# Kernel optimization log

Hardware: AMD Instinct MI355X
Metric: run time of the kernel (lower is better)

The kernel has to match this reference:

```python
import jax, jax.numpy as jnp
import numpy as np

N_NODES = 100000
N_EDGES = 1600000
IN_F = 128
OUT_F = 64
BN_EPS = 1e-5


def setup_inputs() -> dict:
    key = jax.random.key(0)
    ks = jax.random.split(key, 6)
    feature = jax.random.normal(ks[0], (N_NODES, IN_F), dtype=jnp.float32)
    src = jax.random.randint(ks[1], (N_EDGES,), 0, N_NODES, dtype=jnp.int32)
    dst = jax.random.randint(ks[2], (N_EDGES,), 0, N_NODES, dtype=jnp.int32)
    W = jax.random.normal(ks[3], (IN_F, OUT_F), dtype=jnp.float32) * 0.05
    b = jnp.zeros((OUT_F,), dtype=jnp.float32)
    res_W = jax.random.normal(ks[4], (IN_F, OUT_F), dtype=jnp.float32) * 0.05
    res_b = jnp.zeros((OUT_F,), dtype=jnp.float32)
    gamma = jnp.ones((OUT_F,), dtype=jnp.float32)
    beta = jnp.zeros((OUT_F,), dtype=jnp.float32)
    return {"feature": feature, "src": src, "dst": dst, "W": W, "b": b,
            "res_W": res_W, "res_b": res_b, "gamma": gamma, "beta": beta,
            "idx": 0}


def _gcn_layer(feature, src, dst, W, b, res_W, res_b, gamma, beta):
    n = feature.shape[0]
    ones = jnp.ones_like(src, dtype=feature.dtype)
    # DGL norm='both': src-side uses out-degree, dst-side uses in-degree,
    # degrees clamped to min 1 (allow_zero_in_degree=True).
    out_deg = jax.ops.segment_sum(ones, src, num_segments=n)
    in_deg = jax.ops.segment_sum(ones, dst, num_segments=n)
    norm_src = jax.lax.rsqrt(jnp.maximum(out_deg, 1.0))  # [N]
    norm_dst = jax.lax.rsqrt(jnp.maximum(in_deg, 1.0))   # [N]

    # in_feats (128) > out_feats (64): DGL multiplies by W before aggregation.
    h = (feature * norm_src[:, None]) @ W                 # [N, OUT_F]
    agg = jax.ops.segment_sum(h[src], dst, num_segments=n)  # [N, OUT_F]
    conv = jax.nn.relu(agg * norm_dst[:, None] + b)

    # residual connection: activation(Linear(feature))
    res = jax.nn.relu(feature @ res_W + res_b)
    y = conv + res

    # BatchNorm1d (training mode, biased variance)
    mean = jnp.mean(y, axis=0)
    var = jnp.mean(jnp.square(y - mean), axis=0)
    y = (y - mean) * jax.lax.rsqrt(var + BN_EPS) * gamma + beta
    return y


def reference(feature, src, dst, W, b, res_W, res_b, gamma, beta, idx):
    # idx == 0 -> dropout branch is skipped (eval-deterministic reference)
    return _gcn_layer(feature, src, dst, W, b, res_W, res_b, gamma, beta)
```

## Files before the change

### kernel.cpp

```cpp
#include <hip/hip_runtime.h>
#include <hip/hip_fp16.h>

#define NCOL 64
#define KDIM 128
#define NB 512
#define CH 2048

typedef short bf16x8 __attribute__((ext_vector_type(8)));
typedef float f32x4 __attribute__((ext_vector_type(4)));
typedef float f32x2 __attribute__((ext_vector_type(2)));

__device__ __forceinline__ unsigned short f2bf(float f) {
    unsigned int u = __float_as_uint(f);
    return (unsigned short)((u + 0x7fffu + ((u >> 16) & 1u)) >> 16);
}

__global__ __launch_bounds__(256) void coarse_hist(const int* __restrict__ dst,
                                                   int* __restrict__ bcnt, int E) {
    __shared__ int lh[NB];
    int tid = threadIdx.x;
    for (int i = tid; i < NB; i += 256) lh[i] = 0;
    __syncthreads();
    int i = blockIdx.x * blockDim.x + tid;
    int stride = gridDim.x * blockDim.x;
    for (int e = i; e < E; e += stride)
        atomicAdd(&lh[dst[e] >> 8], 1);
    __syncthreads();
    for (int k = tid; k < NB; k += 256) {
        int c = lh[k];
        if (c) atomicAdd(&bcnt[k], c);
    }
}

__global__ __launch_bounds__(256) void bucket_scan(const int* __restrict__ bcnt,
                                                   int* __restrict__ bbase, int* __restrict__ bcur,
                                                   int* __restrict__ row_start, int N, int E) {
    __shared__ int wsum[8];
    int tid = threadIdx.x, lane = tid & 63, wv = tid >> 6;
    int a = bcnt[tid], b = bcnt[tid + 256];
    int ia = a, ib = b;
#pragma unroll
    for (int off = 1; off < 64; off <<= 1) {
        int t = __shfl_up(ia, off); if (lane >= off) ia += t;
        int u = __shfl_up(ib, off); if (lane >= off) ib += u;
    }
    if (lane == 63) { wsum[wv] = ia; wsum[4 + wv] = ib; }
    __syncthreads();
    if (tid == 0) { int run = 0; for (int i = 0; i < 8; ++i) { int t = wsum[i]; wsum[i] = run; run += t; } }
    __syncthreads();
    int ea = wsum[wv] + ia - a;
    int eb = wsum[4 + wv] + ib - b;
    bbase[tid] = ea; bcur[tid] = ea;
    bbase[tid + 256] = eb; bcur[tid + 256] = eb;
    if (tid == 0) row_start[N] = E;
}

__global__ __launch_bounds__(256) void partition_kernel(
    const int* __restrict__ src, const int* __restrict__ dst,
    int* __restrict__ bcur, unsigned int* __restrict__ pk,
    int* __restrict__ outcnt, int E) {
    __shared__ int hist[NB];
    __shared__ int lbase[NB];
    __shared__ int gbase[NB];
    __shared__ int lcur[NB];
    __shared__ uint2 sp[CH];
    __shared__ int wsum[8];

    int tid = threadIdx.x, lane = tid & 63, wv = tid >> 6;
    int c0 = blockIdx.x * CH;
    int cnt = min(CH, E - c0);

    for (int i = tid; i < NB; i += 256) hist[i] = 0;
    __syncthreads();
    for (int i = tid; i < cnt; i += 256)
        atomicAdd(&hist[dst[c0 + i] >> 8], 1);
    __syncthreads();

    {
        int a = hist[tid], b = hist[tid + 256];
        int ia = a, ib = b;
#pragma unroll
        for (int off = 1; off < 64; off <<= 1) {
            int t = __shfl_up(ia, off); if (lane >= off) ia += t;
            int u = __shfl_up(ib, off); if (lane >= off) ib += u;
        }
        if (lane == 63) { wsum[wv] = ia; wsum[4 + wv] = ib; }
        __syncthreads();
        if (tid == 0) { int run = 0; for (int i = 0; i < 8; ++i) { int t = wsum[i]; wsum[i] = run; run += t; } }
        __syncthreads();
        lbase[tid] = wsum[wv] + ia - a;
        lbase[tid + 256] = wsum[4 + wv] + ib - b;
    }
    __syncthreads();

    for (int k = tid; k < NB; k += 256) {
        int c = hist[k];
        gbase[k] = c ? atomicAdd(&bcur[k], c) : 0;
        lcur[k] = lbase[k];
    }
    __syncthreads();

    for (int i = tid; i < cnt; i += 256) {
        int s = src[c0 + i], d = dst[c0 + i];
        atomicAdd(&outcnt[s], 1);
        int p = atomicAdd(&lcur[d >> 8], 1);
        sp[p] = make_uint2((unsigned)s, (unsigned)d);
    }
    __syncthreads();

    for (int i = tid; i < cnt; i += 256) {
        uint2 p = sp[i];
        int k = (int)(p.y >> 8);
        pk[gbase[k] + (i - lbase[k])] = ((p.y & 255u) << 17) | p.x;
    }
}

__global__ __launch_bounds__(256) void fine_kernel(
    const unsigned int* __restrict__ pk, const int* __restrict__ bbase,
    int* __restrict__ row_start, int* __restrict__ ssrc, int E, int nbuck, int N) {
    __shared__ int hist[256];
    __shared__ int cur[256];
    __shared__ int wsum[4];
    int k = blockIdx.x;
    int tid = threadIdx.x, lane = tid & 63, wv = tid >> 6;
    int b0 = bbase[k];
    int b1 = (k + 1 < nbuck) ? bbase[k + 1] : E;

    hist[tid] = 0;
    __syncthreads();
    for (int i = b0 + tid; i < b1; i += 256)
        atomicAdd(&hist[pk[i] >> 17], 1);
    __syncthreads();

    int x = hist[tid], inc = x;
#pragma unroll
    for (int off = 1; off < 64; off <<= 1) {
        int t = __shfl_up(inc, off); if (lane >= off) inc += t;
    }
    if (lane == 63) wsum[wv] = inc;
    __syncthreads();
    if (tid == 0) { int run = 0; for (int i = 0; i < 4; ++i) { int t = wsum[i]; wsum[i] = run; run += t; } }
    __syncthreads();
    int excl = wsum[wv] + inc - x;

    int d = (k << 8) + tid;
    if (d < N) row_start[d] = b0 + excl;
    cur[tid] = b0 + excl;
    __syncthreads();

    for (int i = b0 + tid; i < b1; i += 256) {
        unsigned int p = pk[i];
        int pos = atomicAdd(&cur[p >> 17], 1);
        ssrc[pos] = (int)(p & 0x1FFFFu);
    }
}

__global__ __launch_bounds__(256) void matmul_mfma(
    const float* __restrict__ feat, const float* __restrict__ W,
    const float* __restrict__ RW, const float* __restrict__ res_b,
    const int* __restrict__ outcnt,
    unsigned int* __restrict__ hb8, float* __restrict__ y, int N) {
    __shared__ bf16x8 Bf[2048];
    int tid = threadIdx.x;
    for (int idx = tid; idx < 2048; idx += 256) {
        int mat = idx >> 10;
        int kc = (idx >> 8) & 3;
        int ct = (idx >> 6) & 3;
        int l = idx & 63;
        const float* Wp = mat ? RW : W;
        int kbase = kc * 32 + (l >> 4) * 8;
        int col = ct * 16 + (l & 15);
        bf16x8 t;
#pragma unroll
        for (int j = 0; j < 8; ++j)
            t[j] = (short)f2bf(Wp[(size_t)(kbase + j) * NCOL + col]);
        Bf[idx] = t;
    }
    __syncthreads();

    int lane = tid & 63;
    int wid = tid >> 6;
    int ntiles = (N + 15) >> 4;
    int tile = blockIdx.x * 4 + wid;
    if (tile >= ntiles) return;
    int c16 = lane & 15, kg = lane >> 4;

    float rbv[4];
#pragma unroll
    for (int ct = 0; ct < 4; ++ct) rbv[ct] = res_b[ct * 16 + c16];

    int tb = tile << 4;
    f32x4 acch[4], accr[4];
#pragma unroll
    for (int ct = 0; ct < 4; ++ct) {
        acch[ct] = (f32x4){0.f, 0.f, 0.f, 0.f};
        accr[ct] = (f32x4){0.f, 0.f, 0.f, 0.f};
    }

    int arow = tb + c16; if (arow >= N) arow = N - 1;
    const float* fp = feat + (size_t)arow * KDIM + kg * 8;
#pragma unroll
    for (int kc = 0; kc < 4; ++kc) {
        float4 a0 = *(const float4*)(fp + kc * 32);
        float4 a1 = *(const float4*)(fp + kc * 32 + 4);
        bf16x8 af;
        af[0] = (short)f2bf(a0.x); af[1] = (short)f2bf(a0.y);
        af[2] = (short)f2bf(a0.z); af[3] = (short)f2bf(a0.w);
        af[4] = (short)f2bf(a1.x); af[5] = (short)f2bf(a1.y);
        af[6] = (short)f2bf(a1.z); af[7] = (short)f2bf(a1.w);
#pragma unroll
        for (int ct = 0; ct < 4; ++ct) {
            acch[ct] = __builtin_amdgcn_mfma_f32_16x16x32_bf16(
                af, Bf[(kc * 4 + ct) * 64 + lane], acch[ct], 0, 0, 0);
            accr[ct] = __builtin_amdgcn_mfma_f32_16x16x32_bf16(
                af, Bf[1024 + (kc * 4 + ct) * 64 + lane], accr[ct], 0, 0, 0);
        }
    }

    float nrm[4];
#pragma unroll
    for (int r = 0; r < 4; ++r) {
        int rw = tb + kg * 4 + r; if (rw >= N) rw = N - 1;
        nrm[r] = rsqrtf(fmaxf((float)outcnt[rw], 1.0f));
    }
#pragma unroll
    for (int r = 0; r < 4; ++r) {
        int row = tb + kg * 4 + r;
        if (row < N) {
            unsigned int p = 0;
            p = (unsigned int)__builtin_amdgcn_cvt_pk_fp8_f32(
                    acch[0][r] * nrm[r], acch[1][r] * nrm[r], (int)p, false);
            p = (unsigned int)__builtin_amdgcn_cvt_pk_fp8_f32(
                    acch[2][r] * nrm[r], acch[3][r] * nrm[r], (int)p, true);
#pragma unroll
            for (int ct = 0; ct < 4; ++ct)
                y[(size_t)row * NCOL + ct * 16 + c16] = fmaxf(accr[ct][r] + rbv[ct], 0.0f);
            hb8[(size_t)row * 16 + c16] = p;
        }
    }
}

#define GATHER_ROW_STEP(eBase, eEnd, A0, A1, A2, A3)                                   \
    {                                                                                   \
        int e0 = (eBase) + e4, e1 = e0 + 4, e2 = e0 + 8, e3 = e0 + 12;                  \
        int i0 = (e0 < (eEnd)) ? ssrc[e0] : -1;                                         \
        int i1 = (e1 < (eEnd)) ? ssrc[e1] : -1;                                         \
        int i2 = (e2 < (eEnd)) ? ssrc[e2] : -1;                                         \
        int i3 = (e3 < (eEnd)) ? ssrc[e3] : -1;                                         \
        unsigned int v0 = (i0 >= 0) ? hb8[(size_t)i0 * 16 + dw] : 0u;                   \
        unsigned int v1 = (i1 >= 0) ? hb8[(size_t)i1 * 16 + dw] : 0u;                   \
        unsigned int v2 = (i2 >= 0) ? hb8[(size_t)i2 * 16 + dw] : 0u;                   \
        unsigned int v3 = (i3 >= 0) ? hb8[(size_t)i3 * 16 + dw] : 0u;                   \
        f32x2 l0 = __builtin_amdgcn_cvt_pk_f32_fp8((int)v0, false);                     \
        f32x2 h0 = __builtin_amdgcn_cvt_pk_f32_fp8((int)v0, true);                      \
        f32x2 l1 = __builtin_amdgcn_cvt_pk_f32_fp8((int)v1, false);                     \
        f32x2 h1 = __builtin_amdgcn_cvt_pk_f32_fp8((int)v1, true);                      \
        f32x2 l2 = __builtin_amdgcn_cvt_pk_f32_fp8((int)v2, false);                     \
        f32x2 h2 = __builtin_amdgcn_cvt_pk_f32_fp8((int)v2, true);                      \
        f32x2 l3 = __builtin_amdgcn_cvt_pk_f32_fp8((int)v3, false);                     \
        f32x2 h3 = __builtin_amdgcn_cvt_pk_f32_fp8((int)v3, true);                      \
        A0 += (l0[0] + l1[0]) + (l2[0] + l3[0]);                                        \
        A1 += (l0[1] + l1[1]) + (l2[1] + l3[1]);                                        \
        A2 += (h0[0] + h1[0]) + (h2[0] + h3[0]);                                        \
        A3 += (h0[1] + h1[1]) + (h2[1] + h3[1]);                                        \
    }

__global__ __launch_bounds__(256) void gather_kernel(
    const int* __restrict__ row_start, const int* __restrict__ ssrc,
    const unsigned int* __restrict__ hb8, const float* __restrict__ b,
    float* __restrict__ y, float* __restrict__ stats, int N) {
    int tid = threadIdx.x, lane = tid & 63, wid = tid >> 6;
    int e4 = lane >> 4, dw = lane & 15;
    int rowSel = e4 >> 1;
    int colLo = ((e4 & 1) << 5) + dw;
    int wave = blockIdx.x * 4 + wid;
    int nwaves = gridDim.x * 4;

    float bcLo = b[colLo], bcHi = b[colLo + 16];
    float bnLo = 0.f, bnHi = 0.f, bnsqLo = 0.f, bnsqHi = 0.f;

    for (int d0 = wave * 2; d0 < N; d0 += 2 * nwaves) {
        int d1 = d0 + 1;
        int a0 = row_start[d0], a1 = row_start[d0 + 1];
        int b0e = 0, b1e = 0;
        if (d1 < N) { b0e = a1; b1e = row_start[d1 + 1]; }

        float A0 = 0.f, A1 = 0.f, A2 = 0.f, A3 = 0.f;
        float B0 = 0.f, B1 = 0.f, B2 = 0.f, B3 = 0.f;
        int nit = max((a1 - a0 + 15) >> 4, (b1e - b0e + 15) >> 4);
        for (int it = 0; it < nit; ++it) {
            GATHER_ROW_STEP(a0 + it * 16, a1, A0, A1, A2, A3)
            GATHER_ROW_STEP(b0e + it * 16, b1e, B0, B1, B2, B3)
        }

#pragma unroll
        for (int off = 16; off <= 32; off <<= 1) {
            A0 += __shfl_xor(A0, off); A1 += __shfl_xor(A1, off);
            A2 += __shfl_xor(A2, off); A3 += __shfl_xor(A3, off);
            B0 += __shfl_xor(B0, off); B1 += __shfl_xor(B1, off);
            B2 += __shfl_xor(B2, off); B3 += __shfl_xor(B3, off);
        }

        int dd = d0 + rowSel;
        if (dd < N) {
            int deg = rowSel ? (b1e - b0e) : (a1 - a0);
            float nd = rsqrtf(fmaxf((float)deg, 1.0f));
            float vLo = rowSel ? ((e4 & 1) ? B2 : B0) : ((e4 & 1) ? A2 : A0);
            float vHi = rowSel ? ((e4 & 1) ? B3 : B1) : ((e4 & 1) ? A3 : A1);
            float* yp = &y[(size_t)dd * NCOL + colLo];
            float v0 = fmaxf(vLo * nd + bcLo, 0.f) + yp[0];
            float v1 = fmaxf(vHi * nd + bcHi, 0.f) + yp[16];
            yp[0] = v0;
            yp[16] = v1;
            bnLo += v0; bnsqLo += v0 * v0;
            bnHi += v1; bnsqHi += v1 * v1;
        }
    }

    bnLo += __shfl_xor(bnLo, 32); bnsqLo += __shfl_xor(bnsqLo, 32);
    bnHi += __shfl_xor(bnHi, 32); bnsqHi += __shfl_xor(bnsqHi, 32);

    __shared__ float bnred[4][128];
    if (lane < 32) {
        bnred[wid][colLo] = bnLo;
        bnred[wid][colLo + 16] = bnHi;
        bnred[wid][64 + colLo] = bnsqLo;
        bnred[wid][64 + colLo + 16] = bnsqHi;
    }
    __syncthreads();
    if (tid < 128) {
        float v = bnred[0][tid] + bnred[1][tid] + bnred[2][tid] + bnred[3][tid];
        unsafeAtomicAdd(&stats[tid], v);
    }
}

__global__ __launch_bounds__(256) void apply_kernel(float* __restrict__ y,
                                                    const float* __restrict__ stats,
                                                    const float* __restrict__ gamma,
                                                    const float* __restrict__ beta,
                                                    float invN, int total4) {
    __shared__ float sc[64], sh[64];
    int tid = threadIdx.x;
    if (tid < 64) {
        float mean = stats[tid] * invN;
        float var = stats[64 + tid] * invN - mean * mean;
        float s = gamma[tid] * rsqrtf(var + 1e-5f);
        sc[tid] = s;
        sh[tid] = beta[tid] - mean * s;
    }
    __syncthreads();
    int i = blockIdx.x * blockDim.x + tid;
    int stride = gridDim.x * blockDim.x;
    float4* y4 = (float4*)y;
    for (; i < total4; i += stride) {
        float4 v = y4[i];
        int cbase = (i & 15) << 2;
        float4 s = *(const float4*)&sc[cbase];
        float4 t = *(const float4*)&sh[cbase];
        v.x = v.x * s.x + t.x;
        v.y = v.y * s.y + t.y;
        v.z = v.z * s.z + t.z;
        v.w = v.w * s.w + t.w;
        y4[i] = v;
    }
}

extern "C" void kernel_launch(void* const* d_in, const int* in_sizes, int n_in,
                              void* d_out, int out_size, void* d_ws, size_t ws_size,
                              hipStream_t stream) {
    const float* feat  = (const float*)d_in[0];
    const int*   src   = (const int*)d_in[1];
    const int*   dst   = (const int*)d_in[2];
    const float* W     = (const float*)d_in[3];
    const float* b     = (const float*)d_in[4];
    const float* RW    = (const float*)d_in[5];
    const float* rb    = (const float*)d_in[6];
    const float* gamma = (const float*)d_in[7];
    const float* beta  = (const float*)d_in[8];

    int N = in_sizes[0] / KDIM;
    int E = in_sizes[1];
    float* out = (float*)d_out;
    int nbuck = (N + 255) >> 8;

    char* wsb = (char*)d_ws;
    unsigned int* hb8 = (unsigned int*)wsb;                wsb += (size_t)N * 16 * 4;
    unsigned int* pk  = (unsigned int*)wsb;                wsb += (size_t)E * 4;
    int*   ssrc     = (int*)wsb;                           wsb += (size_t)E * 4;
    int*   row_start= (int*)wsb;                           wsb += (size_t)(N + 1) * 4;
    int*   outcnt   = (int*)wsb;                           wsb += (size_t)N * 4;
    float* stats    = (float*)wsb;                         wsb += 256 * 4;
    int*   bcnt     = (int*)wsb;                           wsb += NB * 4;
    int*   bbase    = (int*)wsb;                           wsb += NB * 4;
    int*   bcur     = (int*)wsb;

    hipMemsetAsync(outcnt, 0, ((size_t)N + 256 + NB) * 4, stream);

    coarse_hist<<<512, 256, 0, stream>>>(dst, bcnt, E);
    bucket_scan<<<1, 256, 0, stream>>>(bcnt, bbase, bcur, row_start, N, E);
    partition_kernel<<<(E + CH - 1) / CH, 256, 0, stream>>>(src, dst, bcur, pk, outcnt, E);
    matmul_mfma<<<(((N + 15) >> 4) + 3) / 4, 256, 0, stream>>>(feat, W, RW, rb, outcnt, hb8, out, N);
    fine_kernel<<<nbuck, 256, 0, stream>>>(pk, bbase, row_start, ssrc, E, nbuck, N);
    gather_kernel<<<2048, 256, 0, stream>>>(row_start, ssrc, hb8, b, out, stats, N);
    apply_kernel<<<2048, 256, 0, stream>>>(out, stats, gamma, beta, 1.0f / (float)N, (N * NCOL) / 4);
}
```

Measured before the change: 263.8 us.

## Replace atomic bucket partition with per-chunk histogram scan and deterministic scatter

The coarse bucket sort is restructured. A chunked histogram kernel now counts out-degrees and per-chunk bucket counts, a per-bucket scan over chunks computes exact offsets, and a scatter kernel writes packed edges directly using LDS cursors. This removes the LDS staging buffer, the global bcur atomics and the in-block scan from the partition step, and the matmul can start right after the histogram. The cost is a chunk-by-bucket global table, an extra scan launch, and uncoalesced global scatter writes instead of staged writes.

```diff
diff --git a/kernel.cpp b/kernel.cpp
--- a/kernel.cpp
+++ b/kernel.cpp
@@ -4,7 +4,7 @@
 #define NCOL 64
 #define KDIM 128
 #define NB 512
-#define CH 2048
+#define CH 4096
 
 typedef short bf16x8 __attribute__((ext_vector_type(8)));
 typedef float f32x4 __attribute__((ext_vector_type(4)));
@@ -15,25 +15,32 @@
     return (unsigned short)((u + 0x7fffu + ((u >> 16) & 1u)) >> 16);
 }
 
-__global__ __launch_bounds__(256) void coarse_hist(const int* __restrict__ dst,
-                                                   int* __restrict__ bcnt, int E) {
+__global__ __launch_bounds__(512) void hist_kernel(const int* __restrict__ src,
+                                                   const int* __restrict__ dst,
+                                                   int* __restrict__ outcnt,
+                                                   int* __restrict__ bcnt,
+                                                   int* __restrict__ gh, int E) {
     __shared__ int lh[NB];
     int tid = threadIdx.x;
-    for (int i = tid; i < NB; i += 256) lh[i] = 0;
-    __syncthreads();
-    int i = blockIdx.x * blockDim.x + tid;
-    int stride = gridDim.x * blockDim.x;
-    for (int e = i; e < E; e += stride)
-        atomicAdd(&lh[dst[e] >> 8], 1);
-    __syncthreads();
-    for (int k = tid; k < NB; k += 256) {
-        int c = lh[k];
-        if (c) atomicAdd(&bcnt[k], c);
+    int c = blockIdx.x;
+    if (tid < NB) lh[tid] = 0;
+    __syncthreads();
+    int c0 = c * CH;
+    int cnt = min(CH, E - c0);
+    for (int i = tid; i < cnt; i += 512) {
+        atomicAdd(&outcnt[src[c0 + i]], 1);
+        atomicAdd(&lh[dst[c0 + i] >> 8], 1);
+    }
+    __syncthreads();
+    if (tid < NB) {
+        int v = lh[tid];
+        gh[(size_t)c * NB + tid] = v;
+        if (v) atomicAdd(&bcnt[tid], v);
     }
 }
 
 __global__ __launch_bounds__(256) void bucket_scan(const int* __restrict__ bcnt,
-                                                   int* __restrict__ bbase, int* __restrict__ bcur,
+                                                   int* __restrict__ bbase,
                                                    int* __restrict__ row_start, int N, int E) {
     __shared__ int wsum[8];
     int tid = threadIdx.x, lane = tid & 63, wv = tid >> 6;
@@ -48,70 +55,58 @@
     __syncthreads();
     if (tid == 0) { int run = 0; for (int i = 0; i < 8; ++i) { int t = wsum[i]; wsum[i] = run; run += t; } }
     __syncthreads();
-    int ea = wsum[wv] + ia - a;
-    int eb = wsum[4 + wv] + ib - b;
-    bbase[tid] = ea; bcur[tid] = ea;
-    bbase[tid + 256] = eb; bcur[tid + 256] = eb;
+    bbase[tid] = wsum[wv] + ia - a;
+    bbase[tid + 256] = wsum[4 + wv] + ib - b;
     if (tid == 0) row_start[N] = E;
 }
 
-__global__ __launch_bounds__(256) void partition_kernel(
-    const int* __restrict__ src, const int* __restrict__ dst,
-    int* __restrict__ bcur, unsigned int* __restrict__ pk,
-    int* __restrict__ outcnt, int E) {
-    __shared__ int hist[NB];
-    __shared__ int lbase[NB];
-    __shared__ int gbase[NB];
+__global__ __launch_bounds__(256) void chunk_scan(int* __restrict__ gh,
+                                                  const int* __restrict__ bbase, int nchunks) {
+    __shared__ int wsum[4];
+    __shared__ int carry_s, tot_s;
+    int k = blockIdx.x;
+    int tid = threadIdx.x, lane = tid & 63, wv = tid >> 6;
+    if (tid == 0) carry_s = bbase[k];
+    __syncthreads();
+    for (int t0 = 0; t0 < nchunks; t0 += 256) {
+        int c = t0 + tid;
+        int x = (c < nchunks) ? gh[(size_t)c * NB + k] : 0;
+        int inc = x;
+#pragma unroll
+        for (int off = 1; off < 64; off <<= 1) {
+            int t = __shfl_up(inc, off); if (lane >= off) inc += t;
+        }
+        if (lane == 63) wsum[wv] = inc;
+        __syncthreads();
+        if (tid == 0) {
+            int run = 0;
+            for (int i = 0; i < 4; ++i) { int t = wsum[i]; wsum[i] = run; run += t; }
+            tot_s = run;
+        }
+        __syncthreads();
+        int excl = carry_s + wsum[wv] + inc - x;
+        if (c < nchunks) gh[(size_t)c * NB + k] = excl;
+        __syncthreads();
+        if (tid == 0) carry_s += tot_s;
+        __syncthreads();
+    }
+}
+
+__global__ __launch_bounds__(512) void scatter_pk(const int* __restrict__ src,
+                                                  const int* __restrict__ dst,
+                                                  const int* __restrict__ gh,
+                                                  unsigned int* __restrict__ pk, int E) {
     __shared__ int lcur[NB];
-    __shared__ uint2 sp[CH];
-    __shared__ int wsum[8];
-
-    int tid = threadIdx.x, lane = tid & 63, wv = tid >> 6;
-    int c0 = blockIdx.x * CH;
+    int tid = threadIdx.x;
+    int c = blockIdx.x;
+    if (tid < NB) lcur[tid] = gh[(size_t)c * NB + tid];
+    __syncthreads();
+    int c0 = c * CH;
     int cnt = min(CH, E - c0);
-
-    for (int i = tid; i < NB; i += 256) hist[i] = 0;
-    __syncthreads();
-    for (int i = tid; i < cnt; i += 256)
-        atomicAdd(&hist[dst[c0 + i] >> 8], 1);
-    __syncthreads();
-
-    {
-        int a = hist[tid], b = hist[tid + 256];
-        int ia = a, ib = b;
-#pragma unroll
-        for (int off = 1; off < 64; off <<= 1) {
-            int t = __shfl_up(ia, off); if (lane >= off) ia += t;
-            int u = __shfl_up(ib, off); if (lane >= off) ib += u;
-        }
-        if (lane == 63) { wsum[wv] = ia; wsum[4 + wv] = ib; }
-        __syncthreads();
-        if (tid == 0) { int run = 0; for (int i = 0; i < 8; ++i) { int t = wsum[i]; wsum[i] = run; run += t; } }
-        __syncthreads();
-        lbase[tid] = wsum[wv] + ia - a;
-        lbase[tid + 256] = wsum[4 + wv] + ib - b;
-    }
-    __syncthreads();
-
-    for (int k = tid; k < NB; k += 256) {
-        int c = hist[k];
-        gbase[k] = c ? atomicAdd(&bcur[k], c) : 0;
-        lcur[k] = lbase[k];
-    }
-    __syncthreads();
-
-    for (int i = tid; i < cnt; i += 256) {
+    for (int i = tid; i < cnt; i += 512) {
         int s = src[c0 + i], d = dst[c0 + i];
-        atomicAdd(&outcnt[s], 1);
-        int p = atomicAdd(&lcur[d >> 8], 1);
-        sp[p] = make_uint2((unsigned)s, (unsigned)d);
-    }
-    __syncthreads();
-
-    for (int i = tid; i < cnt; i += 256) {
-        uint2 p = sp[i];
-        int k = (int)(p.y >> 8);
-        pk[gbase[k] + (i - lbase[k])] = ((p.y & 255u) << 17) | p.x;
+        int pos = atomicAdd(&lcur[d >> 8], 1);
+        pk[pos] = ((unsigned)(d & 255) << 17) | (unsigned)s;
     }
 }
 
@@ -382,6 +377,7 @@
     int E = in_sizes[1];
     float* out = (float*)d_out;
     int nbuck = (N + 255) >> 8;
+    int nchunks = (E + CH - 1) / CH;
 
     char* wsb = (char*)d_ws;
     unsigned int* hb8 = (unsigned int*)wsb;                wsb += (size_t)N * 16 * 4;
@@ -392,14 +388,15 @@
     float* stats    = (float*)wsb;                         wsb += 256 * 4;
     int*   bcnt     = (int*)wsb;                           wsb += NB * 4;
     int*   bbase    = (int*)wsb;                           wsb += NB * 4;
-    int*   bcur     = (int*)wsb;
+    int*   gh       = (int*)wsb;
 
     hipMemsetAsync(outcnt, 0, ((size_t)N + 256 + NB) * 4, stream);
 
-    coarse_hist<<<512, 256, 0, stream>>>(dst, bcnt, E);
-    bucket_scan<<<1, 256, 0, stream>>>(bcnt, bbase, bcur, row_start, N, E);
-    partition_kernel<<<(E + CH - 1) / CH, 256, 0, stream>>>(src, dst, bcur, pk, outcnt, E);
+    hist_kernel<<<nchunks, 512, 0, stream>>>(src, dst, outcnt, bcnt, gh, E);
+    bucket_scan<<<1, 256, 0, stream>>>(bcnt, bbase, row_start, N, E);
     matmul_mfma<<<(((N + 15) >> 4) + 3) / 4, 256, 0, stream>>>(feat, W, RW, rb, outcnt, hb8, out, N);
+    chunk_scan<<<NB, 256, 0, stream>>>(gh, bbase, nchunks);
+    scatter_pk<<<nchunks, 512, 0, stream>>>(src, dst, gh, pk, E);
     fine_kernel<<<nbuck, 256, 0, stream>>>(pk, bbase, row_start, ssrc, E, nbuck, N);
     gather_kernel<<<2048, 256, 0, stream>>>(row_start, ssrc, hb8, b, out, stats, N);
     apply_kernel<<<2048, 256, 0, stream>>>(out, stats, gamma, beta, 1.0f / (float)N, (N * NCOL) / 4);
```

Result: faster. 239.1 us (-9.4%).
